# Performance work log

Measured on AMD Instinct MI355X. Metric: run time of the kernel, lower is better.

The kernel has to match this reference:

```python
import jax, jax.numpy as jnp
import numpy as np

B = 128
D = 128            # d_model
LENS = [512, 256, 128, 64]   # finest -> coarsest level lengths
ORDERS = [1, 2, 3, 4]        # front_block order, then front_blocks[0..2] orders


def freq_interp(x, target_len):
    # x: (B, C, L_in) -> (B, C, target_len). Zero-pad spectrum, scale by len ratio.
    l_in = x.shape[2]
    xf = jnp.fft.rfft(x, axis=2)                                  # (B,C,l_in//2+1)
    pad = target_len // 2 + 1 - xf.shape[2]
    of = jnp.pad(xf, ((0, 0), (0, 0), (0, pad)))
    out = jnp.fft.irfft(of, n=target_len, axis=2)
    return out * (l_in / target_len)


def cheby_kan(x, coeffs):
    # x: (B,N,C_in), coeffs: (C_in, C_out, deg+1). T_k(t) = cos(k*acos(t)).
    deg1 = coeffs.shape[2]
    theta = jnp.arccos(jnp.tanh(jnp.tanh(x)))                     # (B,N,C_in)
    basis = jnp.cos(theta[..., None] * jnp.arange(deg1, dtype=x.dtype))  # (B,N,C_in,deg+1)
    return jnp.einsum('bnid,iod->bno', basis, coeffs)


def dw_conv(x, w):
    # depthwise Conv1d, kernel 3, padding 1, no bias. x: (B,N,C), w: (C,3).
    xc = jnp.transpose(x, (0, 2, 1))                              # (B,C,N)
    k = w[:, None, :]                                             # (C,1,3) OIH
    y = jax.lax.conv_general_dilated(
        xc, k, window_strides=(1,), padding=[(1, 1)],
        dimension_numbers=('NCH', 'OIH', 'NCH'),
        feature_group_count=x.shape[2])
    return jnp.transpose(y, (0, 2, 1))


def m_kan(x, coeffs, w):
    return cheby_kan(x, coeffs) + dw_conv(x, w)


def setup_inputs():
    key = jax.random.key(0)
    ks = jax.random.split(key, 16)
    inp = {}
    for i, L in enumerate(LENS):
        inp[f'x{i}'] = jax.random.normal(ks[i], (B, L, D), dtype=jnp.float32)
    for j, order in enumerate(ORDERS):
        std = 1.0 / (D * (order + 1))
        inp[f'coeffs{j}'] = std * jax.random.normal(ks[4 + 2 * j], (D, D, order + 1), dtype=jnp.float32)
        inp[f'w{j}'] = 0.1 * jax.random.normal(ks[5 + 2 * j], (D, 3), dtype=jnp.float32)
    return inp


def reference(x0, x1, x2, x3,
              coeffs0, w0, coeffs1, w1, coeffs2, w2, coeffs3, w3):
    levels = [x0, x1, x2, x3]
    rev_lens = LENS[::-1]                      # [64, 128, 256, 512]

    # ---- FrequencyDecomp ----
    rev = levels[::-1]
    out_low, out_high = rev[0], rev[1]
    dec = [out_low]
    for i in range(len(rev) - 1):
        res = jnp.transpose(
            freq_interp(jnp.transpose(out_low, (0, 2, 1)), rev_lens[i + 1]), (0, 2, 1))
        dec.append(out_high - res)
        out_low = out_high
        if i + 2 <= len(rev) - 1:
            out_high = rev[i + 2]
    dec = dec[::-1]

    # ---- FrequencyMixing ----
    rev = dec[::-1]
    out_low = m_kan(rev[0], coeffs0, w0)       # front_block, order=begin_order
    out_high = rev[1]
    blocks = [(coeffs1, w1), (coeffs2, w2), (coeffs3, w3)]
    mix = [out_low]
    for i in range(len(rev) - 1):
        oh = m_kan(out_high, *blocks[i])
        res = jnp.transpose(
            freq_interp(jnp.transpose(out_low, (0, 2, 1)), rev_lens[i + 1]), (0, 2, 1))
        out_low = oh + res
        mix.append(out_low)
        if i + 2 <= len(rev) - 1:
            out_high = rev[i + 2]
    mix = mix[::-1]
    return tuple(mix)
```

## Files before the change

kernel.cpp:

```cpp
#include <hip/hip_runtime.h>
#include <math.h>

typedef __attribute__((ext_vector_type(8))) short bf16x8;
typedef __attribute__((ext_vector_type(4))) float f32x4;

__device__ __forceinline__ unsigned short f2bf(float f) {
    unsigned u = __float_as_uint(f);
    unsigned r = (u + 0x7FFF + ((u >> 16) & 1)) >> 16;
    return (unsigned short)r;
}

__device__ __forceinline__ float fast_tanh(float x) {
    float e2 = __builtin_amdgcn_exp2f(x * 2.885390081777927f);
    return fmaf(-2.0f, __builtin_amdgcn_rcpf(e2 + 1.0f), 1.0f);
}

__device__ __forceinline__ void gload_lds16(const unsigned short* g,
                                            unsigned short* l) {
    __builtin_amdgcn_global_load_lds(
        (const __attribute__((address_space(1))) unsigned int*)g,
        (__attribute__((address_space(3))) unsigned int*)l, 16, 0, 0);
}

__device__ __forceinline__ void castT_tile(
    const float* __restrict__ src, unsigned short* __restrict__ dst,
    int b, int n0, int L)
{
    __shared__ unsigned short tt[128][72];
    const int tid = threadIdx.x;
    for (int i = tid; i < 64 * 32; i += 256) {
        int nr = i >> 5, c4 = (i & 31) * 4;
        float4 v = *(const float4*)(src + ((size_t)b * L + n0 + nr) * 128 + c4);
        tt[c4 + 0][nr] = f2bf(v.x);
        tt[c4 + 1][nr] = f2bf(v.y);
        tt[c4 + 2][nr] = f2bf(v.z);
        tt[c4 + 3][nr] = f2bf(v.w);
    }
    __syncthreads();
    const int c = tid >> 1, seg = (tid & 1) * 32;
    unsigned short* dp = dst + ((size_t)b * 128 + c) * L + n0 + seg;
    #pragma unroll
    for (int j = 0; j < 32; j += 8)
        *(bf16x8*)(dp + j) = *(const bf16x8*)&tt[c][seg + j];
}

__global__ __launch_bounds__(256) void prep_all(
    const float* __restrict__ x1, const float* __restrict__ x2,
    const float* __restrict__ x3,
    unsigned short* __restrict__ Xt1, unsigned short* __restrict__ Xt2,
    unsigned short* __restrict__ Xt3,
    unsigned short* __restrict__ U256, unsigned short* __restrict__ U128,
    unsigned short* __restrict__ U64p,
    const float* __restrict__ c0, const float* __restrict__ c1,
    const float* __restrict__ c2, const float* __restrict__ c3,
    unsigned short* __restrict__ BmT_all, float* __restrict__ bias_all)
{
    const int bid = blockIdx.x, tid = threadIdx.x;
    if (bid < 896) {
        if (bid < 512)      castT_tile(x1, Xt1, bid >> 2, (bid & 3) * 64, 256);
        else if (bid < 768) castT_tile(x2, Xt2, (bid - 512) >> 1, ((bid - 512) & 1) * 64, 128);
        else                castT_tile(x3, Xt3, bid - 768, 0, 64);
    } else if (bid < 1568) {
        int fid = (bid - 896) * 256 + tid;
        unsigned short* U; int L, lg, e;
        if (fid < 131072)      { U = U256; L = 256; lg = 8; e = fid; }
        else if (fid < 163840) { U = U128; L = 128; lg = 7; e = fid - 131072; }
        else                   { U = U64p; L = 64;  lg = 6; e = fid - 163840; }
        const int n = e & (L - 1);
        const int m = e >> lg;
        const int t = m >> 1;
        const float inv4L = 1.0f / (4.0f * (float)L);
        float val;
        if ((m & 1) == 0) {
            val = ((t == n) ? 0.25f : 0.0f) + (((t + n) & 1) ? -inv4L : inv4L);
        } else {
            int idx = (t - n) & (L - 1);
            double th = M_PI * (2.0 * idx + 1.0) / (2.0 * L);
            double ct = cos(th) / sin(th);
            val = (float)((idx & 1) ? -ct : ct) * inv4L;
        }
        U[e] = f2bf(val);
    } else {
        const int r   = bid - 1568;
        const int set = r >> 6;
        const int o   = ((r & 63) << 1) + (tid >> 7);
        const int i   = tid & 127;
        const int DEG1 = set + 2;
        const float* cc = (set == 0) ? c0 : (set == 1) ? c1 : (set == 2) ? c2 : c3;
        const float* cp = cc + ((size_t)i * 128 + o) * DEG1;
        unsigned short* Bm = BmT_all + (size_t)set * 65536;
        for (int d = 1; d < DEG1; ++d)
            Bm[(size_t)(d - 1) * 16384 + o * 128 + i] = f2bf(cp[d]);
        float s = cp[0];
        #pragma unroll
        for (int off = 32; off >= 1; off >>= 1) s += __shfl_down(s, off);
        __shared__ float red[4];
        if ((tid & 63) == 0) red[tid >> 6] = s;
        __syncthreads();
        if ((tid & 127) == 0)
            bias_all[set * 128 + o] = red[tid >> 6] + red[(tid >> 6) + 1];
    }
}

__device__ __forceinline__ void up2_body(
    const unsigned short* __restrict__ U,
    const unsigned short* __restrict__ Xt,
    const float* __restrict__ xh,
    float* __restrict__ out,
    unsigned short* __restrict__ xtm,
    float sign, int b, int mt, int L)
{
    const int NK = L >> 5;
    const int tid = threadIdx.x;
    __shared__ unsigned short Ab[2][2048];
    __shared__ unsigned short Bb[2][4096];

    const int ln = tid & 63, wv = tid >> 6;
    const int wm = wv & 1, wn = wv >> 1;
    const int lr = ln & 15, qd = ln >> 4;

    f32x4 acc[2][4];
    #pragma unroll
    for (int mi = 0; mi < 2; ++mi)
        #pragma unroll
        for (int nt = 0; nt < 4; ++nt)
            acc[mi][nt] = (f32x4){0.f, 0.f, 0.f, 0.f};

    const int arow = tid >> 2, acol = (tid & 3) * 8;

    auto stage = [&](int kk, int buf) {
        const unsigned short* ga = U + (size_t)(mt * 64 + arow) * L + kk * 32 + acol;
        gload_lds16(ga, (unsigned short*)Ab[buf] + (tid << 3));
        #pragma unroll
        for (int j = 0; j < 2; ++j) {
            int sidx = tid + (j << 8);
            const unsigned short* gb =
                Xt + ((size_t)b * 128 + (sidx >> 2)) * L + kk * 32 + (sidx & 3) * 8;
            gload_lds16(gb, (unsigned short*)Bb[buf] + (sidx << 3));
        }
    };

    stage(0, 0);
    for (int kk = 0; kk < NK; ++kk) {
        __syncthreads();
        if (kk + 1 < NK) stage(kk + 1, (kk + 1) & 1);
        const int buf = kk & 1;
        bf16x8 af[2], bfv[4];
        #pragma unroll
        for (int mi = 0; mi < 2; ++mi)
            af[mi] = *(const bf16x8*)&Ab[buf][(wm * 32 + mi * 16 + lr) * 32 + qd * 8];
        #pragma unroll
        for (int nt = 0; nt < 4; ++nt)
            bfv[nt] = *(const bf16x8*)&Bb[buf][(wn * 64 + nt * 16 + lr) * 32 + qd * 8];
        #pragma unroll
        for (int mi = 0; mi < 2; ++mi)
            #pragma unroll
            for (int nt = 0; nt < 4; ++nt)
                acc[mi][nt] = __builtin_amdgcn_mfma_f32_16x16x32_bf16(
                    af[mi], bfv[nt], acc[mi][nt], 0, 0, 0);
    }

    const int twoL = L << 1;
    #pragma unroll
    for (int nt = 0; nt < 4; ++nt) {
        const int col = wn * 64 + nt * 16 + lr;
        #pragma unroll
        for (int mi = 0; mi < 2; ++mi) {
            #pragma unroll
            for (int r = 0; r < 4; ++r) {
                const int row = mt * 64 + wm * 32 + mi * 16 + qd * 4 + r;
                const size_t gi = ((size_t)b * twoL + row) * 128 + col;
                float v = xh[gi] + sign * acc[mi][nt][r];
                out[gi] = v;
                if (xtm)
                    xtm[((size_t)b * 128 + col) * twoL + row] = f2bf(v);
            }
        }
    }
}

__global__ __launch_bounds__(256) void up2_dec(
    const unsigned short* __restrict__ U64p, const unsigned short* __restrict__ U128,
    const unsigned short* __restrict__ U256,
    const unsigned short* __restrict__ Xt3, const unsigned short* __restrict__ Xt2,
    const unsigned short* __restrict__ Xt1,
    const float* __restrict__ x2, const float* __restrict__ x1,
    const float* __restrict__ x0,
    float* __restrict__ d2, float* __restrict__ d1, float* __restrict__ d0)
{
    const int bid = blockIdx.x;
    const unsigned short *U, *Xt; const float* xh; float* out;
    int L, lgMT, base;
    if (bid < 256)      { U = U64p; Xt = Xt3; xh = x2; out = d2; L = 64;  lgMT = 1; base = 0; }
    else if (bid < 768) { U = U128; Xt = Xt2; xh = x1; out = d1; L = 128; lgMT = 2; base = 256; }
    else                { U = U256; Xt = Xt1; xh = x0; out = d0; L = 256; lgMT = 3; base = 768; }
    const int rb = bid - base;
    up2_body(U, Xt, xh, out, nullptr, -1.f, rb >> lgMT, rb & ((1 << lgMT) - 1), L);
}

__global__ __launch_bounds__(256) void up2_mix(
    const unsigned short* __restrict__ U, const unsigned short* __restrict__ Xt,
    float* __restrict__ m, unsigned short* __restrict__ xtm, int L, int lgMT)
{
    up2_body(U, Xt, m, m, xtm, 1.f,
             blockIdx.x >> lgMT, blockIdx.x & ((1 << lgMT) - 1), L);
}

__global__ __launch_bounds__(256) void mkan_all(
    const float* __restrict__ xa, const float* __restrict__ xb,
    const float* __restrict__ xc, const float* __restrict__ xd,
    const unsigned short* __restrict__ BmT_all,
    const float* __restrict__ bias_all,
    const float* __restrict__ w0p, const float* __restrict__ w1p,
    const float* __restrict__ w2p, const float* __restrict__ w3p,
    float* __restrict__ m0, float* __restrict__ m1,
    float* __restrict__ m2, float* __restrict__ m3,
    unsigned short* __restrict__ xtm0)
{
    __shared__ float Us[32][132];
    __shared__ unsigned short Bb[2][4096];

    const int bid = blockIdx.x, tid = threadIdx.x;
    const float *x, *w; float* outp; unsigned short* xtm = nullptr;
    int set, mb, Lmask;
    if (bid < 256)       { x = xa; w = w0p; outp = m0; set = 0; mb = bid << 5;          Lmask = 63;  xtm = xtm0; }
    else if (bid < 768)  { x = xb; w = w1p; outp = m1; set = 1; mb = (bid - 256) << 5;  Lmask = 127; }
    else if (bid < 1792) { x = xc; w = w2p; outp = m2; set = 2; mb = (bid - 768) << 5;  Lmask = 255; }
    else                 { x = xd; w = w3p; outp = m3; set = 3; mb = (bid - 1792) << 5; Lmask = 511; }
    const int deg1m1 = set + 1;
    const int NK = deg1m1 << 2;
    const unsigned short* Bm = BmT_all + (size_t)set * 65536;
    const float* bias = bias_all + (set << 7);

    auto stageB = [&](int p, int c4, int buf) {
        const int i0 = c4 << 5;
        #pragma unroll
        for (int j = 0; j < 2; ++j) {
            int sidx = tid + (j << 8);
            const unsigned short* gb =
                Bm + (size_t)((p << 7) + (sidx >> 2)) * 128 + i0 + ((sidx & 3) << 3);
            gload_lds16(gb, (unsigned short*)Bb[buf] + (sidx << 3));
        }
    };

    stageB(0, 0, 0);

    for (int e = tid * 4; e < 4096; e += 1024) {
        const int row = e >> 7, i = e & 127;
        float4 v = *(const float4*)(x + ((size_t)(mb + row)) * 128 + i);
        float4 r;
        r.x = fast_tanh(fast_tanh(v.x));
        r.y = fast_tanh(fast_tanh(v.y));
        r.z = fast_tanh(fast_tanh(v.z));
        r.w = fast_tanh(fast_tanh(v.w));
        *(float4*)&Us[row][i] = r;
    }

    const int ln = tid & 63, wv = tid >> 6;
    const int wm = wv & 1, wn = wv >> 1;
    const int lr = ln & 15, qd = ln >> 4;
    const int arow = (wm << 4) + lr;

    f32x4 acc[4];
    #pragma unroll
    for (int nt = 0; nt < 4; ++nt) acc[nt] = (f32x4){0.f, 0.f, 0.f, 0.f};

    __syncthreads();

    int s = 0;
    for (int c4 = 0; c4 < 4; ++c4) {
        const float4 ua = *(const float4*)&Us[arow][(c4 << 5) + (qd << 3)];
        const float4 ub = *(const float4*)&Us[arow][(c4 << 5) + (qd << 3) + 4];
        const float u0 = ua.x, u1 = ua.y, u2 = ua.z, u3 = ua.w;
        const float u4 = ub.x, u5 = ub.y, u6 = ub.z, u7 = ub.w;
        float tp0 = 1.f, tp1 = 1.f, tp2 = 1.f, tp3 = 1.f;
        float tp4 = 1.f, tp5 = 1.f, tp6 = 1.f, tp7 = 1.f;
        float tc0 = u0, tc1 = u1, tc2 = u2, tc3 = u3;
        float tc4 = u4, tc5 = u5, tc6 = u6, tc7 = u7;
        for (int p = 0; p < deg1m1; ++p, ++s) {
            if (s) __syncthreads();
            if (s + 1 < NK) {
                int np = p + 1, nc4 = c4;
                if (np == deg1m1) { np = 0; ++nc4; }
                stageB(np, nc4, (s + 1) & 1);
            }
            union { unsigned int w[4]; bf16x8 v; } afu;
            asm("v_cvt_pk_bf16_f32 %0, %1, %2" : "=v"(afu.w[0]) : "v"(tc0), "v"(tc1));
            asm("v_cvt_pk_bf16_f32 %0, %1, %2" : "=v"(afu.w[1]) : "v"(tc2), "v"(tc3));
            asm("v_cvt_pk_bf16_f32 %0, %1, %2" : "=v"(afu.w[2]) : "v"(tc4), "v"(tc5));
            asm("v_cvt_pk_bf16_f32 %0, %1, %2" : "=v"(afu.w[3]) : "v"(tc6), "v"(tc7));
            const int buf = s & 1;
            bf16x8 bfv[4];
            #pragma unroll
            for (int nt = 0; nt < 4; ++nt)
                bfv[nt] = *(const bf16x8*)&Bb[buf][(((wn << 6) + (nt << 4) + lr) << 5) + (qd << 3)];
            #pragma unroll
            for (int nt = 0; nt < 4; ++nt)
                acc[nt] = __builtin_amdgcn_mfma_f32_16x16x32_bf16(afu.v, bfv[nt], acc[nt], 0, 0, 0);
            float tn;
            tn = fmaf(2.f * u0, tc0, -tp0); tp0 = tc0; tc0 = tn;
            tn = fmaf(2.f * u1, tc1, -tp1); tp1 = tc1; tc1 = tn;
            tn = fmaf(2.f * u2, tc2, -tp2); tp2 = tc2; tc2 = tn;
            tn = fmaf(2.f * u3, tc3, -tp3); tp3 = tc3; tc3 = tn;
            tn = fmaf(2.f * u4, tc4, -tp4); tp4 = tc4; tc4 = tn;
            tn = fmaf(2.f * u5, tc5, -tp5); tp5 = tc5; tc5 = tn;
            tn = fmaf(2.f * u6, tc6, -tp6); tp6 = tc6; tc6 = tn;
            tn = fmaf(2.f * u7, tc7, -tp7); tp7 = tc7; tc7 = tn;
        }
    }

    #pragma unroll
    for (int nt = 0; nt < 4; ++nt) {
        const int col = (wn << 6) + (nt << 4) + lr;
        const float ww0 = w[col * 3 + 0], ww1 = w[col * 3 + 1], ww2 = w[col * 3 + 2];
        const float bs = bias[col];
        #pragma unroll
        for (int r = 0; r < 4; ++r) {
            const int row = (wm << 4) + (qd << 2) + r;
            const int gm = mb + row;
            const int n = gm & Lmask;
            const size_t gi = (size_t)gm * 128 + col;
            float xm1 = (n > 0)     ? x[gi - 128] : 0.f;
            float x0v = x[gi];
            float xp1 = (n < Lmask) ? x[gi + 128] : 0.f;
            float v = acc[nt][r] + bs + fmaf(ww0, xm1, fmaf(ww1, x0v, ww2 * xp1));
            outp[gi] = v;
            if (xtm)
                xtm[(size_t)(((gm >> 6) << 7) + col) * 64 + (gm & 63)] = f2bf(v);
        }
    }
}

extern "C" void kernel_launch(void* const* d_in, const int* in_sizes, int n_in,
                              void* d_out, int out_size, void* d_ws, size_t ws_size,
                              hipStream_t stream) {
    const float* x0 = (const float*)d_in[0];
    const float* x1 = (const float*)d_in[1];
    const float* x2 = (const float*)d_in[2];
    const float* x3 = (const float*)d_in[3];
    const float* c0 = (const float*)d_in[4];
    const float* w0 = (const float*)d_in[5];
    const float* c1 = (const float*)d_in[6];
    const float* w1 = (const float*)d_in[7];
    const float* c2 = (const float*)d_in[8];
    const float* w2 = (const float*)d_in[9];
    const float* c3 = (const float*)d_in[10];
    const float* w3 = (const float*)d_in[11];
    float* out = (float*)d_out;

    float* d0 = (float*)d_ws;
    float* d1 = d0 + 8388608;
    float* d2 = d1 + 4194304;
    unsigned short* Xt1  = (unsigned short*)(d2 + 2097152);
    unsigned short* Xt2  = Xt1 + 4194304;
    unsigned short* Xt3  = Xt2 + 2097152;
    unsigned short* Xtm0 = Xt3 + 1048576;
    unsigned short* Xtm1 = Xtm0 + 1048576;
    unsigned short* Xtm2 = Xtm1 + 2097152;
    unsigned short* BmT  = Xtm2 + 4194304;
    float* bias_all = (float*)(BmT + 262144);
    unsigned short* U256 = (unsigned short*)(bias_all + 512);
    unsigned short* U128 = U256 + 131072;
    unsigned short* U64p = U128 + 32768;

    float* m3 = out;
    float* m2 = m3 + 8388608;
    float* m1 = m2 + 4194304;
    float* m0 = m1 + 2097152;

    prep_all<<<1824, 256, 0, stream>>>(x1, x2, x3, Xt1, Xt2, Xt3,
                                       U256, U128, U64p,
                                       c0, c1, c2, c3, BmT, bias_all);

    up2_dec<<<1792, 256, 0, stream>>>(U64p, U128, U256, Xt3, Xt2, Xt1,
                                      x2, x1, x0, d2, d1, d0);

    mkan_all<<<3840, 256, 0, stream>>>(x3, d2, d1, d0, BmT, bias_all,
                                       w0, w1, w2, w3, m0, m1, m2, m3, Xtm0);

    up2_mix<<<256,  256, 0, stream>>>(U64p, Xtm0, m1, Xtm1, 64, 1);
    up2_mix<<<512,  256, 0, stream>>>(U128, Xtm1, m2, Xtm2, 128, 2);
    up2_mix<<<1024, 256, 0, stream>>>(U256, Xtm2, m3, nullptr, 256, 3);
}
```

Measured before the change: 264.5 us.

## Fuse mixing-stage upsample GEMM into per-level m-KAN kernels

The single merged m-KAN launch followed by three upsample-add launches is replaced by a dedicated kernel for the coarsest level plus a chained kernel per finer level. Each chained kernel accumulates the Chebyshev-KAN GEMM and the frequency-interpolation GEMM into the same MFMA accumulators and writes the output once. This removes the fp32 read-modify-write of m1..m3 and the separate upsample launches. In exchange, the per-level work becomes a serial chain of launches, where before all four levels ran concurrently in one kernel, and each block has a longer K loop and uses smaller 32-row upsample tiles.

```diff
diff --git a/kernel.cpp b/kernel.cpp
--- a/kernel.cpp
+++ b/kernel.cpp
@@ -107,8 +107,7 @@
     const unsigned short* __restrict__ Xt,
     const float* __restrict__ xh,
     float* __restrict__ out,
-    unsigned short* __restrict__ xtm,
-    float sign, int b, int mt, int L)
+    int b, int mt, int L)
 {
     const int NK = L >> 5;
     const int tid = threadIdx.x;
@@ -170,10 +169,7 @@
             for (int r = 0; r < 4; ++r) {
                 const int row = mt * 64 + wm * 32 + mi * 16 + qd * 4 + r;
                 const size_t gi = ((size_t)b * twoL + row) * 128 + col;
-                float v = xh[gi] + sign * acc[mi][nt][r];
-                out[gi] = v;
-                if (xtm)
-                    xtm[((size_t)b * 128 + col) * twoL + row] = f2bf(v);
+                out[gi] = xh[gi] - acc[mi][nt][r];
             }
         }
     }
@@ -195,44 +191,122 @@
     else if (bid < 768) { U = U128; Xt = Xt2; xh = x1; out = d1; L = 128; lgMT = 2; base = 256; }
     else                { U = U256; Xt = Xt1; xh = x0; out = d0; L = 256; lgMT = 3; base = 768; }
     const int rb = bid - base;
-    up2_body(U, Xt, xh, out, nullptr, -1.f, rb >> lgMT, rb & ((1 << lgMT) - 1), L);
-}
-
-__global__ __launch_bounds__(256) void up2_mix(
-    const unsigned short* __restrict__ U, const unsigned short* __restrict__ Xt,
-    float* __restrict__ m, unsigned short* __restrict__ xtm, int L, int lgMT)
-{
-    up2_body(U, Xt, m, m, xtm, 1.f,
-             blockIdx.x >> lgMT, blockIdx.x & ((1 << lgMT) - 1), L);
-}
-
-__global__ __launch_bounds__(256) void mkan_all(
-    const float* __restrict__ xa, const float* __restrict__ xb,
-    const float* __restrict__ xc, const float* __restrict__ xd,
-    const unsigned short* __restrict__ BmT_all,
-    const float* __restrict__ bias_all,
-    const float* __restrict__ w0p, const float* __restrict__ w1p,
-    const float* __restrict__ w2p, const float* __restrict__ w3p,
-    float* __restrict__ m0, float* __restrict__ m1,
-    float* __restrict__ m2, float* __restrict__ m3,
-    unsigned short* __restrict__ xtm0)
+    up2_body(U, Xt, xh, out, rb >> lgMT, rb & ((1 << lgMT) - 1), L);
+}
+
+__global__ __launch_bounds__(256) void mkan0(
+    const float* __restrict__ x, const unsigned short* __restrict__ Bm,
+    const float* __restrict__ bias, const float* __restrict__ w,
+    float* __restrict__ m0, unsigned short* __restrict__ xtm0)
 {
     __shared__ float Us[32][132];
     __shared__ unsigned short Bb[2][4096];
-
     const int bid = blockIdx.x, tid = threadIdx.x;
-    const float *x, *w; float* outp; unsigned short* xtm = nullptr;
-    int set, mb, Lmask;
-    if (bid < 256)       { x = xa; w = w0p; outp = m0; set = 0; mb = bid << 5;          Lmask = 63;  xtm = xtm0; }
-    else if (bid < 768)  { x = xb; w = w1p; outp = m1; set = 1; mb = (bid - 256) << 5;  Lmask = 127; }
-    else if (bid < 1792) { x = xc; w = w2p; outp = m2; set = 2; mb = (bid - 768) << 5;  Lmask = 255; }
-    else                 { x = xd; w = w3p; outp = m3; set = 3; mb = (bid - 1792) << 5; Lmask = 511; }
-    const int deg1m1 = set + 1;
-    const int NK = deg1m1 << 2;
-    const unsigned short* Bm = BmT_all + (size_t)set * 65536;
-    const float* bias = bias_all + (set << 7);
-
-    auto stageB = [&](int p, int c4, int buf) {
+    const int mb = bid << 5;
+
+    auto stageB = [&](int c4, int buf) {
+        const int i0 = c4 << 5;
+        #pragma unroll
+        for (int j = 0; j < 2; ++j) {
+            int sidx = tid + (j << 8);
+            const unsigned short* gb =
+                Bm + (size_t)(sidx >> 2) * 128 + i0 + ((sidx & 3) << 3);
+            gload_lds16(gb, (unsigned short*)Bb[buf] + (sidx << 3));
+        }
+    };
+
+    stageB(0, 0);
+
+    for (int e = tid * 4; e < 4096; e += 1024) {
+        const int row = e >> 7, i = e & 127;
+        float4 v = *(const float4*)(x + ((size_t)(mb + row)) * 128 + i);
+        float4 r;
+        r.x = fast_tanh(fast_tanh(v.x));
+        r.y = fast_tanh(fast_tanh(v.y));
+        r.z = fast_tanh(fast_tanh(v.z));
+        r.w = fast_tanh(fast_tanh(v.w));
+        *(float4*)&Us[row][i] = r;
+    }
+
+    const int ln = tid & 63, wv = tid >> 6;
+    const int wm = wv & 1, wn = wv >> 1;
+    const int lr = ln & 15, qd = ln >> 4;
+    const int arow = (wm << 4) + lr;
+
+    f32x4 acc[4];
+    #pragma unroll
+    for (int nt = 0; nt < 4; ++nt) acc[nt] = (f32x4){0.f, 0.f, 0.f, 0.f};
+
+    __syncthreads();
+
+    for (int c4 = 0; c4 < 4; ++c4) {
+        if (c4) __syncthreads();
+        if (c4 + 1 < 4) stageB(c4 + 1, (c4 + 1) & 1);
+        const float4 ua = *(const float4*)&Us[arow][(c4 << 5) + (qd << 3)];
+        const float4 ub = *(const float4*)&Us[arow][(c4 << 5) + (qd << 3) + 4];
+        union { unsigned int w[4]; bf16x8 v; } afu;
+        asm("v_cvt_pk_bf16_f32 %0, %1, %2" : "=v"(afu.w[0]) : "v"(ua.x), "v"(ua.y));
+        asm("v_cvt_pk_bf16_f32 %0, %1, %2" : "=v"(afu.w[1]) : "v"(ua.z), "v"(ua.w));
+        asm("v_cvt_pk_bf16_f32 %0, %1, %2" : "=v"(afu.w[2]) : "v"(ub.x), "v"(ub.y));
+        asm("v_cvt_pk_bf16_f32 %0, %1, %2" : "=v"(afu.w[3]) : "v"(ub.z), "v"(ub.w));
+        const int buf = c4 & 1;
+        bf16x8 bfv[4];
+        #pragma unroll
+        for (int nt = 0; nt < 4; ++nt)
+            bfv[nt] = *(const bf16x8*)&Bb[buf][(((wn << 6) + (nt << 4) + lr) << 5) + (qd << 3)];
+        #pragma unroll
+        for (int nt = 0; nt < 4; ++nt)
+            acc[nt] = __builtin_amdgcn_mfma_f32_16x16x32_bf16(afu.v, bfv[nt], acc[nt], 0, 0, 0);
+    }
+
+    #pragma unroll
+    for (int nt = 0; nt < 4; ++nt) {
+        const int col = (wn << 6) + (nt << 4) + lr;
+        const float ww0 = w[col * 3 + 0], ww1 = w[col * 3 + 1], ww2 = w[col * 3 + 2];
+        const float bs = bias[col];
+        #pragma unroll
+        for (int r = 0; r < 4; ++r) {
+            const int row = (wm << 4) + (qd << 2) + r;
+            const int gm = mb + row;
+            const int n = gm & 63;
+            const size_t gi = (size_t)gm * 128 + col;
+            float xm1 = (n > 0)  ? x[gi - 128] : 0.f;
+            float x0v = x[gi];
+            float xp1 = (n < 63) ? x[gi + 128] : 0.f;
+            float v = acc[nt][r] + bs + fmaf(ww0, xm1, fmaf(ww1, x0v, ww2 * xp1));
+            m0[gi] = v;
+            xtm0[(size_t)(((gm >> 6) << 7) + col) * 64 + n] = f2bf(v);
+        }
+    }
+}
+
+__global__ __launch_bounds__(256) void chain_up(
+    const float* __restrict__ x,
+    const unsigned short* __restrict__ Bm,
+    const float* __restrict__ bias,
+    const float* __restrict__ w,
+    const unsigned short* __restrict__ U,
+    const unsigned short* __restrict__ Xtm_in,
+    float* __restrict__ mout,
+    unsigned short* __restrict__ xtm_out,
+    int deg1m1, int lgL)
+{
+    __shared__ float Us[32][132];
+    __shared__ unsigned short Ab[2][1024];
+    __shared__ unsigned short Bb[2][4096];
+
+    const int tid = threadIdx.x;
+    const int mtsh = lgL - 5;
+    const int b  = blockIdx.x >> mtsh;
+    const int mt = blockIdx.x & ((1 << mtsh) - 1);
+    const int L  = 1 << lgL;
+    const int Ku = L >> 1;
+    const int NKc = deg1m1 << 2;
+    const int NKu = Ku >> 5;
+    const int NT  = NKc + NKu;
+    const int mbflat = (b << lgL) + (mt << 5);
+
+    auto stageB_ch = [&](int p, int c4, int buf) {
         const int i0 = c4 << 5;
         #pragma unroll
         for (int j = 0; j < 2; ++j) {
@@ -242,12 +316,26 @@
             gload_lds16(gb, (unsigned short*)Bb[buf] + (sidx << 3));
         }
     };
-
-    stageB(0, 0, 0);
+    auto stage_up = [&](int kk, int buf) {
+        if (tid < 128) {
+            const unsigned short* ga =
+                U + (size_t)((mt << 5) + (tid >> 2)) * Ku + kk * 32 + (tid & 3) * 8;
+            gload_lds16(ga, (unsigned short*)Ab[buf] + (tid << 3));
+        }
+        #pragma unroll
+        for (int j = 0; j < 2; ++j) {
+            int sidx = tid + (j << 8);
+            const unsigned short* gb =
+                Xtm_in + ((size_t)b * 128 + (sidx >> 2)) * Ku + kk * 32 + (sidx & 3) * 8;
+            gload_lds16(gb, (unsigned short*)Bb[buf] + (sidx << 3));
+        }
+    };
+
+    stageB_ch(0, 0, 0);
 
     for (int e = tid * 4; e < 4096; e += 1024) {
         const int row = e >> 7, i = e & 127;
-        float4 v = *(const float4*)(x + ((size_t)(mb + row)) * 128 + i);
+        float4 v = *(const float4*)(x + ((size_t)(mbflat + row)) * 128 + i);
         float4 r;
         r.x = fast_tanh(fast_tanh(v.x));
         r.y = fast_tanh(fast_tanh(v.y));
@@ -279,10 +367,12 @@
         float tc4 = u4, tc5 = u5, tc6 = u6, tc7 = u7;
         for (int p = 0; p < deg1m1; ++p, ++s) {
             if (s) __syncthreads();
-            if (s + 1 < NK) {
+            if (s + 1 < NKc) {
                 int np = p + 1, nc4 = c4;
                 if (np == deg1m1) { np = 0; ++nc4; }
-                stageB(np, nc4, (s + 1) & 1);
+                stageB_ch(np, nc4, (s + 1) & 1);
+            } else if (s + 1 < NT) {
+                stage_up(0, (s + 1) & 1);
             }
             union { unsigned int w[4]; bf16x8 v; } afu;
             asm("v_cvt_pk_bf16_f32 %0, %1, %2" : "=v"(afu.w[0]) : "v"(tc0), "v"(tc1));
@@ -309,6 +399,21 @@
         }
     }
 
+    for (int kk = 0; kk < NKu; ++kk, ++s) {
+        __syncthreads();
+        if (kk + 1 < NKu) stage_up(kk + 1, (s + 1) & 1);
+        const int buf = s & 1;
+        bf16x8 af = *(const bf16x8*)&Ab[buf][((wm << 4) + lr) * 32 + (qd << 3)];
+        bf16x8 bfv[4];
+        #pragma unroll
+        for (int nt = 0; nt < 4; ++nt)
+            bfv[nt] = *(const bf16x8*)&Bb[buf][(((wn << 6) + (nt << 4) + lr) << 5) + (qd << 3)];
+        #pragma unroll
+        for (int nt = 0; nt < 4; ++nt)
+            acc[nt] = __builtin_amdgcn_mfma_f32_16x16x32_bf16(af, bfv[nt], acc[nt], 0, 0, 0);
+    }
+
+    const int Lmask = L - 1;
     #pragma unroll
     for (int nt = 0; nt < 4; ++nt) {
         const int col = (wn << 6) + (nt << 4) + lr;
@@ -316,17 +421,16 @@
         const float bs = bias[col];
         #pragma unroll
         for (int r = 0; r < 4; ++r) {
-            const int row = (wm << 4) + (qd << 2) + r;
-            const int gm = mb + row;
-            const int n = gm & Lmask;
+            const int nloc = (mt << 5) + (wm << 4) + (qd << 2) + r;
+            const int gm = (b << lgL) + nloc;
             const size_t gi = (size_t)gm * 128 + col;
-            float xm1 = (n > 0)     ? x[gi - 128] : 0.f;
+            float xm1 = (nloc > 0)     ? x[gi - 128] : 0.f;
             float x0v = x[gi];
-            float xp1 = (n < Lmask) ? x[gi + 128] : 0.f;
+            float xp1 = (nloc < Lmask) ? x[gi + 128] : 0.f;
             float v = acc[nt][r] + bs + fmaf(ww0, xm1, fmaf(ww1, x0v, ww2 * xp1));
-            outp[gi] = v;
-            if (xtm)
-                xtm[(size_t)(((gm >> 6) << 7) + col) * 64 + (gm & 63)] = f2bf(v);
+            mout[gi] = v;
+            if (xtm_out)
+                xtm_out[((size_t)b * 128 + col) * L + nloc] = f2bf(v);
         }
     }
 }
@@ -375,10 +479,12 @@
     up2_dec<<<1792, 256, 0, stream>>>(U64p, U128, U256, Xt3, Xt2, Xt1,
                                       x2, x1, x0, d2, d1, d0);
 
-    mkan_all<<<3840, 256, 0, stream>>>(x3, d2, d1, d0, BmT, bias_all,
-                                       w0, w1, w2, w3, m0, m1, m2, m3, Xtm0);
-
-    up2_mix<<<256,  256, 0, stream>>>(U64p, Xtm0, m1, Xtm1, 64, 1);
-    up2_mix<<<512,  256, 0, stream>>>(U128, Xtm1, m2, Xtm2, 128, 2);
-    up2_mix<<<1024, 256, 0, stream>>>(U256, Xtm2, m3, nullptr, 256, 3);
-}
+    mkan0<<<256, 256, 0, stream>>>(x3, BmT, bias_all, w0, m0, Xtm0);
+
+    chain_up<<<512, 256, 0, stream>>>(d2, BmT + 65536, bias_all + 128, w1,
+                                      U64p, Xtm0, m1, Xtm1, 2, 7);
+    chain_up<<<1024, 256, 0, stream>>>(d1, BmT + 131072, bias_all + 256, w2,
+                                       U128, Xtm1, m2, Xtm2, 3, 8);
+    chain_up<<<2048, 256, 0, stream>>>(d0, BmT + 196608, bias_all + 384, w3,
+                                       U256, Xtm2, m3, nullptr, 4, 9);
+}
```

Result: slower. 283.0 us (+7.0%).
